# Optimization experiments

Hardware: AMD Instinct MI355X
Metric: run time of the kernel (lower is better)

Reference implementation:

```python
import jax, jax.numpy as jnp
import numpy as np

BW_MIN, BW_MAX, FLOAT_AMT, NEG_SLOPE = 0.1, 0.5, 0.1, 0.1


def setup_inputs() -> dict:
    key = jax.random.key(0)
    ks = jax.random.split(key, 24)
    B, S, IN_CH, GRID_CH, IC, DIR, OUT_CH = 8, 2000, 120, 64, 512, 4, 2
    NUM_BLOCK = 8
    n_layers = NUM_BLOCK - 2  # 6
    # grid coordinates: meshgrid over [0,10) with gap 0.1 -> 100x100 = 10000 pts
    gx = np.arange(0.0, 10.0, 0.1)
    gy = np.arange(0.0, 10.0, 0.1)
    GX, GY = np.meshgrid(gx, gy)
    grid_coors_xy = jnp.asarray(np.stack([GX.flatten(), GY.flatten()], axis=1), dtype=jnp.float32)  # [N,2]
    N = grid_coors_xy.shape[0]
    cat_ch = IN_CH + 2 * GRID_CH  # 248
    inp = {
        'input_stuff': jax.random.normal(ks[0], (B, S, IN_CH), jnp.float32),
        'sound_loc': jax.random.uniform(ks[1], (B, 4), jnp.float32) * 10.0,  # inside grid extent
        'grid_coors_xy': grid_coors_xy,
        'xy_offset': jnp.zeros((N, 2), jnp.float32),
        'bandwidths': jnp.full((N,), 0.25, jnp.float32),
        'grid_0': jax.random.normal(ks[2], (N, GRID_CH), jnp.float32) / np.sqrt(float(GRID_CH)),
        'proj_W': jax.random.normal(ks[3], (cat_ch, IC), jnp.float32) / np.sqrt(float(cat_ch)),
        'proj_b': jnp.zeros((IC,), jnp.float32),
        'res_W0': jax.random.normal(ks[4], (cat_ch, IC), jnp.float32) / np.sqrt(float(cat_ch)),
        'res_b0': jnp.zeros((IC,), jnp.float32),
        'res_W1': jax.random.normal(ks[5], (IC, IC), jnp.float32) / np.sqrt(float(IC)),
        'res_b1': jnp.zeros((IC,), jnp.float32),
        'layers_W': jax.random.normal(ks[6], (n_layers, IC, IC), jnp.float32) / np.sqrt(float(IC)),
        'layers_b': jnp.zeros((n_layers, IC), jnp.float32),
        'channels': jax.random.normal(ks[7], (NUM_BLOCK - 1, DIR, IC), jnp.float32) / np.sqrt(float(IC)),
        'out_W': jax.random.normal(ks[8], (IC, OUT_CH), jnp.float32) / np.sqrt(float(IC)),
        'out_b': jnp.zeros((OUT_CH,), jnp.float32),
    }
    return inp


def _leaky(x):
    return jax.nn.leaky_relu(x, NEG_SLOPE)


def _fit_predict(grid_pos, grid_feat, query_pos, bandwidths):
    d2 = jnp.sum((query_pos[:, None, :] - grid_pos[None, :, :]) ** 2, axis=-1)  # [B,N]
    w = jnp.exp(-d2 / (bandwidths[None, :] ** 2))                               # [B,N]
    w = w / jnp.sum(w, axis=-1, keepdims=True)
    return w @ grid_feat                                                        # [B,F]


def reference(input_stuff, sound_loc, grid_coors_xy, xy_offset, bandwidths, grid_0,
              proj_W, proj_b, res_W0, res_b0, res_W1, res_b1,
              layers_W, layers_b, channels, out_W, out_b):
    B, S = input_stuff.shape[0], input_stuff.shape[1]
    bw = jnp.clip(bandwidths, BW_MIN, BW_MAX)
    grid_baseline = grid_coors_xy + jnp.tanh(xy_offset) * FLOAT_AMT
    feat0 = _fit_predict(grid_baseline, grid_0, sound_loc[:, :2], bw)  # [B,64]
    feat1 = _fit_predict(grid_baseline, grid_0, sound_loc[:, 2:], bw)  # [B,64]
    total_grid = jnp.concatenate([feat0, feat1], axis=-1)              # [B,128]
    total_grid = jnp.broadcast_to(total_grid[:, None, :], (B, S, total_grid.shape[-1]))
    my_input = jnp.concatenate([total_grid, input_stuff], axis=-1)     # [B,S,248]

    # proj then broadcast over direction channels + learned channel embedding
    out = (my_input @ proj_W + proj_b)[:, :, None, :] + channels[0][None, None]  # [B,S,4,512]

    n_layers = layers_W.shape[0]
    half = n_layers // 2 - 1
    for k in range(n_layers):
        out = _leaky(out) @ layers_W[k] + layers_b[k] + channels[k + 1][None, None]
        if k == half:
            r = _leaky(my_input @ res_W0 + res_b0) @ res_W1 + res_b1  # [B,S,512]
            out = out + r[:, :, None, :]
    return out @ out_W + out_b  # [B,S,4,2]
```

## Files before the change

kernel.cpp:

```cpp
#include <hip/hip_runtime.h>
#include <hip/hip_bf16.h>

#define BB 8
#define SS 2000
#define IN_CH 120
#define GRID_CH 64
#define NPTS 10000
#define IC 512
#define DIRS 4
#define CATCH 248
#define CATPAD 256
#define NLAY 6
#define MROWS 16000
#define MROWS4 64000
#define NSLICE 16
#define PTS_PER_SLICE 625

typedef __bf16 bf16x8 __attribute__((ext_vector_type(8)));
typedef float f32x4 __attribute__((ext_vector_type(4)));

#define DEVI __device__ __forceinline__

DEVI unsigned short f2bf(float f) {
    __hip_bfloat16 h = __float2bfloat16(f);
    return __builtin_bit_cast(unsigned short, h);
}
DEVI float bf2f(unsigned short u) {
    unsigned int x = ((unsigned int)u) << 16;
    return __builtin_bit_cast(float, x);
}
DEVI float leaky(float x) { return x > 0.f ? x : 0.1f * x; }

DEVI void gload16(const void* g, void* l) {
    __builtin_amdgcn_global_load_lds(
        (const unsigned int __attribute__((address_space(1)))*)g,
        (unsigned int __attribute__((address_space(3)))*)l, 16, 0, 0);
}

static const size_t OFF_FEATS  = 0;
static const size_t OFF_PROJWT = 4096;
static const size_t OFF_RES0WT = 266240;
static const size_t OFF_RES1WT = 528384;
static const size_t OFF_LAYWT  = 1052672;
static const size_t OFF_MYIN   = 4198400;
static const size_t OFF_R0     = 12390400;
static const size_t OFF_R      = 28774400;
static const size_t OFF_A0     = 45158400;
static const size_t OFF_A1     = 110694400;

__global__ void wconv_k(const float* __restrict__ src, unsigned short* __restrict__ dst,
                        int K, int Kpad, int N, int total) {
    int idx = blockIdx.x * 256 + threadIdx.x;
    if (idx >= total) return;
    int k = idx % Kpad;
    int rem = idx / Kpad;
    int n = rem % N;
    int l = rem / N;
    float v = (k < K) ? src[((size_t)l * K + k) * N + n] : 0.f;
    dst[idx] = f2bf(v);
}

__global__ __launch_bounds__(256) void feats_part_k(
    const float* __restrict__ gxy, const float* __restrict__ goff,
    const float* __restrict__ bws, const float* __restrict__ g0,
    const float* __restrict__ sloc, float* __restrict__ partial) {
    int bq = blockIdx.x;
    int b = bq >> 1, q = bq & 1;
    float qx = sloc[b * 4 + q * 2 + 0];
    float qy = sloc[b * 4 + q * 2 + 1];
    int i0 = blockIdx.y * PTS_PER_SLICE;
    int iend = i0 + PTS_PER_SLICE;
    float swt = 0.f;
    float sf[64];
#pragma unroll
    for (int c = 0; c < 64; c++) sf[c] = 0.f;
    for (int i = i0 + threadIdx.x; i < iend; i += 256) {
        float gx = gxy[i * 2 + 0] + tanhf(goff[i * 2 + 0]) * 0.1f;
        float gy = gxy[i * 2 + 1] + tanhf(goff[i * 2 + 1]) * 0.1f;
        float bw = fminf(fmaxf(bws[i], 0.1f), 0.5f);
        float dx = qx - gx, dy = qy - gy;
        float w = expf(-(dx * dx + dy * dy) / (bw * bw));
        swt += w;
#pragma unroll
        for (int c = 0; c < 64; c++) sf[c] += w * g0[(size_t)i * 64 + c];
    }
#pragma unroll
    for (int c = 0; c < 64; c++)
        for (int o = 32; o; o >>= 1) sf[c] += __shfl_down(sf[c], o);
    for (int o = 32; o; o >>= 1) swt += __shfl_down(swt, o);
    __shared__ float red[4][65];
    int lane = threadIdx.x & 63, wv = threadIdx.x >> 6;
    if (lane == 0) {
#pragma unroll
        for (int c = 0; c < 64; c++) red[wv][c] = sf[c];
        red[wv][64] = swt;
    }
    __syncthreads();
    size_t base = (size_t)(blockIdx.y * 16 + bq) * 72;
    if (threadIdx.x < 64) {
        int c = threadIdx.x;
        partial[base + c] = red[0][c] + red[1][c] + red[2][c] + red[3][c];
        if (c == 0)
            partial[base + 64] = red[0][64] + red[1][64] + red[2][64] + red[3][64];
    }
}

__global__ __launch_bounds__(128) void feats_reduce_k(
    const float* __restrict__ partial, float* __restrict__ feats) {
    int bq = blockIdx.x;
    __shared__ float s[66];
    int t = threadIdx.x;
    if (t < 65) {
        float acc = 0.f;
        for (int sl = 0; sl < NSLICE; ++sl)
            acc += partial[(size_t)(sl * 16 + bq) * 72 + t];
        s[t] = acc;
    }
    __syncthreads();
    if (t < 64) {
        int b = bq >> 1, q = bq & 1;
        feats[b * 128 + q * 64 + t] = s[t] / s[64];
    }
}

__global__ void build_k(const float* __restrict__ feats, const float* __restrict__ inp,
                        unsigned short* __restrict__ dst) {
    int idx = blockIdx.x * 256 + threadIdx.x;
    int c = idx & 255;
    int m = idx >> 8;
    int b = m / SS;
    float v;
    if (c < 128) v = feats[b * 128 + c];
    else if (c < CATCH) v = inp[(size_t)m * IN_CH + (c - 128)];
    else v = 0.f;
    dst[idx] = f2bf(v);
}

template <int EPI>
__global__ __launch_bounds__(256) void gemm_k(
    const unsigned short* __restrict__ A, const unsigned short* __restrict__ BT,
    unsigned short* __restrict__ out, int K,
    const float* __restrict__ bias, const float* __restrict__ chan,
    const unsigned short* __restrict__ resid) {
    __shared__ unsigned short ldsA[8192];
    __shared__ unsigned short ldsB[8192];
    const int tid = threadIdx.x;
    const int lane = tid & 63, wv = tid >> 6;
    const int wm = wv >> 1, wn = wv & 1;
    const int c8 = lane >> 4;
    const int fr = lane & 15;

    int aoff[4][2], boff[4][2];
#pragma unroll
    for (int i = 0; i < 4; i++) {
        int ra = wm * 64 + i * 16 + fr;
        int rb = wn * 64 + i * 16 + fr;
#pragma unroll
        for (int h = 0; h < 2; h++) {
            int c = c8 + h * 4;
            aoff[i][h] = ra * 64 + ((c ^ (ra & 7)) << 3);
            boff[i][h] = rb * 64 + ((c ^ (rb & 7)) << 3);
        }
    }
    int ldso[4];
    size_t asrc[4];
    const unsigned short* Ab = A + (size_t)blockIdx.x * 128 * K;
    const unsigned short* Bb = BT + (size_t)blockIdx.y * 128 * K;
#pragma unroll
    for (int t = 0; t < 4; t++) {
        int o = t * 4096 + wv * 1024 + lane * 16;
        int r = o >> 7;
        int s = (o >> 4) & 7;
        int g = (s ^ (r & 7)) << 3;
        ldso[t] = o >> 1;
        asrc[t] = (size_t)r * K + g;
    }

    f32x4 acc[4][4];
#pragma unroll
    for (int i = 0; i < 4; i++)
#pragma unroll
        for (int j = 0; j < 4; j++) acc[i][j] = (f32x4)0.f;

    const int nK = K >> 6;
    for (int kt = 0; kt < nK; ++kt) {
        const int k0 = kt << 6;
        __syncthreads();
#pragma unroll
        for (int t = 0; t < 4; t++) gload16(Ab + asrc[t] + k0, &ldsA[ldso[t]]);
#pragma unroll
        for (int t = 0; t < 4; t++) gload16(Bb + asrc[t] + k0, &ldsB[ldso[t]]);
        __syncthreads();
#pragma unroll
        for (int h = 0; h < 2; h++) {
            bf16x8 av[4], bv[4];
#pragma unroll
            for (int i = 0; i < 4; i++) av[i] = *(const bf16x8*)&ldsA[aoff[i][h]];
#pragma unroll
            for (int j = 0; j < 4; j++) bv[j] = *(const bf16x8*)&ldsB[boff[j][h]];
#pragma unroll
            for (int i = 0; i < 4; i++)
#pragma unroll
                for (int j = 0; j < 4; j++)
                    acc[i][j] = __builtin_amdgcn_mfma_f32_16x16x32_bf16(av[i], bv[j], acc[i][j], 0, 0, 0);
        }
    }

    const int rbase = (lane >> 4) << 2;
    const size_t m0 = (size_t)blockIdx.x * 128;
    const int n0 = blockIdx.y * 128;
#pragma unroll
    for (int i = 0; i < 4; i++) {
#pragma unroll
        for (int j = 0; j < 4; j++) {
#pragma unroll
            for (int rg = 0; rg < 4; ++rg) {
                size_t m = m0 + wm * 64 + i * 16 + rbase + rg;
                int n = n0 + wn * 64 + j * 16 + fr;
                float v = acc[i][j][rg];
                if constexpr (EPI == 0) {
                    float v0 = v + bias[n];
#pragma unroll
                    for (int d = 0; d < 4; ++d) {
                        float u = v0 + chan[d * 512 + n];
                        out[(m * 4 + d) * 512 + n] = f2bf(leaky(u));
                    }
                } else if constexpr (EPI == 1 || EPI == 2 || EPI == 3) {
                    int d = (int)(m & 3);
                    float u = v + bias[n] + chan[d * 512 + n];
                    if constexpr (EPI == 2) u += bf2f(resid[(m >> 2) * 512 + n]);
                    out[m * 512 + n] = f2bf(EPI == 3 ? u : leaky(u));
                } else {
                    float u = v + bias[n];
                    out[m * 512 + n] = f2bf(EPI == 4 ? leaky(u) : u);
                }
            }
        }
    }
}

__global__ __launch_bounds__(256) void final_k(
    const unsigned short* __restrict__ A, const float* __restrict__ outW,
    const float* __restrict__ outb, float* __restrict__ out) {
    int gw = blockIdx.x * 4 + (threadIdx.x >> 6);
    int lane = threadIdx.x & 63;
    const unsigned short* row = A + (size_t)gw * 512;
    uint4 bits = *(const uint4*)(row + lane * 8);
    unsigned int ww[4] = {bits.x, bits.y, bits.z, bits.w};
    float s0 = 0.f, s1 = 0.f;
#pragma unroll
    for (int j = 0; j < 8; j++) {
        unsigned short u = (unsigned short)((ww[j >> 1] >> ((j & 1) * 16)) & 0xffff);
        float a = bf2f(u);
        int k = lane * 8 + j;
        s0 = fmaf(a, outW[k * 2 + 0], s0);
        s1 = fmaf(a, outW[k * 2 + 1], s1);
    }
    for (int o = 32; o; o >>= 1) {
        s0 += __shfl_down(s0, o);
        s1 += __shfl_down(s1, o);
    }
    if (lane == 0) {
        out[(size_t)gw * 2 + 0] = s0 + outb[0];
        out[(size_t)gw * 2 + 1] = s1 + outb[1];
    }
}

extern "C" void kernel_launch(void* const* d_in, const int* in_sizes, int n_in,
                              void* d_out, int out_size, void* d_ws, size_t ws_size,
                              hipStream_t stream) {
    const float* input_stuff = (const float*)d_in[0];
    const float* sound_loc   = (const float*)d_in[1];
    const float* grid_xy     = (const float*)d_in[2];
    const float* xy_offset   = (const float*)d_in[3];
    const float* bandwidths  = (const float*)d_in[4];
    const float* grid_0      = (const float*)d_in[5];
    const float* proj_W      = (const float*)d_in[6];
    const float* proj_b      = (const float*)d_in[7];
    const float* res_W0      = (const float*)d_in[8];
    const float* res_b0      = (const float*)d_in[9];
    const float* res_W1      = (const float*)d_in[10];
    const float* res_b1      = (const float*)d_in[11];
    const float* layers_W    = (const float*)d_in[12];
    const float* layers_b    = (const float*)d_in[13];
    const float* channels    = (const float*)d_in[14];
    const float* out_W       = (const float*)d_in[15];
    const float* out_b       = (const float*)d_in[16];

    char* ws = (char*)d_ws;
    float* feats            = (float*)(ws + OFF_FEATS);
    unsigned short* projWT  = (unsigned short*)(ws + OFF_PROJWT);
    unsigned short* res0WT  = (unsigned short*)(ws + OFF_RES0WT);
    unsigned short* res1WT  = (unsigned short*)(ws + OFF_RES1WT);
    unsigned short* layWT   = (unsigned short*)(ws + OFF_LAYWT);
    unsigned short* myin    = (unsigned short*)(ws + OFF_MYIN);
    unsigned short* R0      = (unsigned short*)(ws + OFF_R0);
    unsigned short* Rb      = (unsigned short*)(ws + OFF_R);
    unsigned short* A0      = (unsigned short*)(ws + OFF_A0);
    unsigned short* A1      = (unsigned short*)(ws + OFF_A1);
    float* partial          = (float*)(ws + OFF_A0);

    wconv_k<<<(512 * 256 + 255) / 256, 256, 0, stream>>>(proj_W, projWT, CATCH, CATPAD, IC, 512 * 256);
    wconv_k<<<(512 * 256 + 255) / 256, 256, 0, stream>>>(res_W0, res0WT, CATCH, CATPAD, IC, 512 * 256);
    wconv_k<<<(512 * 512 + 255) / 256, 256, 0, stream>>>(res_W1, res1WT, IC, IC, IC, 512 * 512);
    wconv_k<<<(6 * 512 * 512 + 255) / 256, 256, 0, stream>>>(layers_W, layWT, IC, IC, IC, 6 * 512 * 512);

    feats_part_k<<<dim3(16, NSLICE), 256, 0, stream>>>(grid_xy, xy_offset, bandwidths, grid_0, sound_loc, partial);
    feats_reduce_k<<<16, 128, 0, stream>>>(partial, feats);
    build_k<<<MROWS, 256, 0, stream>>>(feats, input_stuff, myin);

    dim3 g16(125, 4), g64(500, 4);
    gemm_k<0><<<g16, 256, 0, stream>>>(myin, projWT, A0, CATPAD, proj_b, channels, nullptr);
    gemm_k<4><<<g16, 256, 0, stream>>>(myin, res0WT, R0, CATPAD, res_b0, nullptr, nullptr);
    gemm_k<5><<<g16, 256, 0, stream>>>(R0, res1WT, Rb, IC, res_b1, nullptr, nullptr);
    gemm_k<1><<<g64, 256, 0, stream>>>(A0, layWT + 0 * 262144, A1, IC, layers_b + 0 * 512, channels + 1 * 2048, nullptr);
    gemm_k<1><<<g64, 256, 0, stream>>>(A1, layWT + 1 * 262144, A0, IC, layers_b + 1 * 512, channels + 2 * 2048, nullptr);
    gemm_k<2><<<g64, 256, 0, stream>>>(A0, layWT + 2 * 262144, A1, IC, layers_b + 2 * 512, channels + 3 * 2048, Rb);
    gemm_k<1><<<g64, 256, 0, stream>>>(A1, layWT + 3 * 262144, A0, IC, layers_b + 3 * 512, channels + 4 * 2048, nullptr);
    gemm_k<1><<<g64, 256, 0, stream>>>(A0, layWT + 4 * 262144, A1, IC, layers_b + 4 * 512, channels + 5 * 2048, nullptr);
    gemm_k<3><<<g64, 256, 0, stream>>>(A1, layWT + 5 * 262144, A0, IC, layers_b + 5 * 512, channels + 6 * 2048, nullptr);

    final_k<<<MROWS, 256, 0, stream>>>(A0, out_W, out_b, (float*)d_out);
}
```

Before: 501.3 us.

## Double-buffer GEMM LDS tiles and remap blocks for XCD-local tile reuse

The GEMM kernel now keeps two LDS buffers so the global-to-LDS load of the next K tile is issued before computing on the current one, leaving one barrier per iteration instead of two. The 2D grid is flattened to 1D and remapped so consecutive logical tiles, which share A rows across the four N tiles, land on the same XCD for better L2 reuse. LDS use doubles to 64KB per block, which may lower occupancy.

```diff
diff --git a/kernel.cpp b/kernel.cpp
--- a/kernel.cpp
+++ b/kernel.cpp
@@ -37,6 +37,15 @@
         (unsigned int __attribute__((address_space(3)))*)l, 16, 0, 0);
 }
 
+DEVI int xcd_swizzle() {
+    int nwg = (int)gridDim.x;
+    int orig = (int)blockIdx.x;
+    int q = nwg >> 3, r = nwg & 7;
+    int xcd = orig & 7, pos = orig >> 3;
+    int base = xcd < r ? xcd * (q + 1) : r * (q + 1) + (xcd - r) * q;
+    return base + pos;
+}
+
 static const size_t OFF_FEATS  = 0;
 static const size_t OFF_PROJWT = 4096;
 static const size_t OFF_RES0WT = 266240;
@@ -142,14 +151,16 @@
     unsigned short* __restrict__ out, int K,
     const float* __restrict__ bias, const float* __restrict__ chan,
     const unsigned short* __restrict__ resid) {
-    __shared__ unsigned short ldsA[8192];
-    __shared__ unsigned short ldsB[8192];
+    __shared__ __align__(16) unsigned short lds[2][2][8192];
     const int tid = threadIdx.x;
     const int lane = tid & 63, wv = tid >> 6;
     const int wm = wv >> 1, wn = wv & 1;
     const int c8 = lane >> 4;
     const int fr = lane & 15;
 
+    const int swz = xcd_swizzle();
+    const int bx = swz >> 2, by = swz & 3;
+
     int aoff[4][2], boff[4][2];
 #pragma unroll
     for (int i = 0; i < 4; i++) {
@@ -164,8 +175,8 @@
     }
     int ldso[4];
     size_t asrc[4];
-    const unsigned short* Ab = A + (size_t)blockIdx.x * 128 * K;
-    const unsigned short* Bb = BT + (size_t)blockIdx.y * 128 * K;
+    const unsigned short* Ab = A + (size_t)bx * 128 * K;
+    const unsigned short* Bb = BT + (size_t)by * 128 * K;
 #pragma unroll
     for (int t = 0; t < 4; t++) {
         int o = t * 4096 + wv * 1024 + lane * 16;
@@ -183,32 +194,47 @@
         for (int j = 0; j < 4; j++) acc[i][j] = (f32x4)0.f;
 
     const int nK = K >> 6;
+#pragma unroll
+    for (int t = 0; t < 4; t++) gload16(Ab + asrc[t], &lds[0][0][ldso[t]]);
+#pragma unroll
+    for (int t = 0; t < 4; t++) gload16(Bb + asrc[t], &lds[0][1][ldso[t]]);
+    asm volatile("s_waitcnt vmcnt(0)" ::: "memory");
+    __builtin_amdgcn_s_barrier();
+    __builtin_amdgcn_sched_barrier(0);
+
+    int buf = 0;
     for (int kt = 0; kt < nK; ++kt) {
-        const int k0 = kt << 6;
-        __syncthreads();
-#pragma unroll
-        for (int t = 0; t < 4; t++) gload16(Ab + asrc[t] + k0, &ldsA[ldso[t]]);
-#pragma unroll
-        for (int t = 0; t < 4; t++) gload16(Bb + asrc[t] + k0, &ldsB[ldso[t]]);
-        __syncthreads();
+        if (kt + 1 < nK) {
+            const int k1 = (kt + 1) << 6;
+#pragma unroll
+            for (int t = 0; t < 4; t++) gload16(Ab + asrc[t] + k1, &lds[buf ^ 1][0][ldso[t]]);
+#pragma unroll
+            for (int t = 0; t < 4; t++) gload16(Bb + asrc[t] + k1, &lds[buf ^ 1][1][ldso[t]]);
+        }
 #pragma unroll
         for (int h = 0; h < 2; h++) {
             bf16x8 av[4], bv[4];
 #pragma unroll
-            for (int i = 0; i < 4; i++) av[i] = *(const bf16x8*)&ldsA[aoff[i][h]];
-#pragma unroll
-            for (int j = 0; j < 4; j++) bv[j] = *(const bf16x8*)&ldsB[boff[j][h]];
+            for (int i = 0; i < 4; i++) av[i] = *(const bf16x8*)&lds[buf][0][aoff[i][h]];
+#pragma unroll
+            for (int j = 0; j < 4; j++) bv[j] = *(const bf16x8*)&lds[buf][1][boff[j][h]];
 #pragma unroll
             for (int i = 0; i < 4; i++)
 #pragma unroll
                 for (int j = 0; j < 4; j++)
                     acc[i][j] = __builtin_amdgcn_mfma_f32_16x16x32_bf16(av[i], bv[j], acc[i][j], 0, 0, 0);
         }
+        if (kt + 1 < nK) {
+            asm volatile("s_waitcnt vmcnt(0)" ::: "memory");
+            __builtin_amdgcn_s_barrier();
+            __builtin_amdgcn_sched_barrier(0);
+        }
+        buf ^= 1;
     }
 
     const int rbase = (lane >> 4) << 2;
-    const size_t m0 = (size_t)blockIdx.x * 128;
-    const int n0 = blockIdx.y * 128;
+    const size_t m0 = (size_t)bx * 128;
+    const int n0 = by * 128;
 #pragma unroll
     for (int i = 0; i < 4; i++) {
 #pragma unroll
@@ -309,16 +335,15 @@
     feats_reduce_k<<<16, 128, 0, stream>>>(partial, feats);
     build_k<<<MROWS, 256, 0, stream>>>(feats, input_stuff, myin);
 
-    dim3 g16(125, 4), g64(500, 4);
-    gemm_k<0><<<g16, 256, 0, stream>>>(myin, projWT, A0, CATPAD, proj_b, channels, nullptr);
-    gemm_k<4><<<g16, 256, 0, stream>>>(myin, res0WT, R0, CATPAD, res_b0, nullptr, nullptr);
-    gemm_k<5><<<g16, 256, 0, stream>>>(R0, res1WT, Rb, IC, res_b1, nullptr, nullptr);
-    gemm_k<1><<<g64, 256, 0, stream>>>(A0, layWT + 0 * 262144, A1, IC, layers_b + 0 * 512, channels + 1 * 2048, nullptr);
-    gemm_k<1><<<g64, 256, 0, stream>>>(A1, layWT + 1 * 262144, A0, IC, layers_b + 1 * 512, channels + 2 * 2048, nullptr);
-    gemm_k<2><<<g64, 256, 0, stream>>>(A0, layWT + 2 * 262144, A1, IC, layers_b + 2 * 512, channels + 3 * 2048, Rb);
-    gemm_k<1><<<g64, 256, 0, stream>>>(A1, layWT + 3 * 262144, A0, IC, layers_b + 3 * 512, channels + 4 * 2048, nullptr);
-    gemm_k<1><<<g64, 256, 0, stream>>>(A0, layWT + 4 * 262144, A1, IC, layers_b + 4 * 512, channels + 5 * 2048, nullptr);
-    gemm_k<3><<<g64, 256, 0, stream>>>(A1, layWT + 5 * 262144, A0, IC, layers_b + 5 * 512, channels + 6 * 2048, nullptr);
+    gemm_k<0><<<500, 256, 0, stream>>>(myin, projWT, A0, CATPAD, proj_b, channels, nullptr);
+    gemm_k<4><<<500, 256, 0, stream>>>(myin, res0WT, R0, CATPAD, res_b0, nullptr, nullptr);
+    gemm_k<5><<<500, 256, 0, stream>>>(R0, res1WT, Rb, IC, res_b1, nullptr, nullptr);
+    gemm_k<1><<<2000, 256, 0, stream>>>(A0, layWT + 0 * 262144, A1, IC, layers_b + 0 * 512, channels + 1 * 2048, nullptr);
+    gemm_k<1><<<2000, 256, 0, stream>>>(A1, layWT + 1 * 262144, A0, IC, layers_b + 1 * 512, channels + 2 * 2048, nullptr);
+    gemm_k<2><<<2000, 256, 0, stream>>>(A0, layWT + 2 * 262144, A1, IC, layers_b + 2 * 512, channels + 3 * 2048, Rb);
+    gemm_k<1><<<2000, 256, 0, stream>>>(A1, layWT + 3 * 262144, A0, IC, layers_b + 3 * 512, channels + 4 * 2048, nullptr);
+    gemm_k<1><<<2000, 256, 0, stream>>>(A0, layWT + 4 * 262144, A1, IC, layers_b + 4 * 512, channels + 5 * 2048, nullptr);
+    gemm_k<3><<<2000, 256, 0, stream>>>(A1, layWT + 5 * 262144, A0, IC, layers_b + 5 * 512, channels + 6 * 2048, nullptr);
 
     final_k<<<MROWS, 256, 0, stream>>>(A0, out_W, out_b, (float*)d_out);
 }
```

Result: faster. 403.8 us (-19.4%).

## Fuse entire MLP chain into one kernel keeping activations in LDS

Applied to the files above, without the earlier changes.

Replaces the build kernel, the nine separate GEMM launches and the final projection with a single fused kernel. Each 512-thread block owns 32 input rows (128 direction rows) and keeps its activation slab in 128KB of swizzled dynamic LDS across all layers. Weights are streamed straight from global or L2 into registers with double buffering, and only the residual branch is written to global memory. This removes the large global round-trips of activations between layers and the per-launch overhead. The cost is one block per CU from LDS usage, heavy register pressure from the 8x4 accumulator tiles, and no LDS reuse of the weight tiles.

```diff
diff --git a/kernel.cpp b/kernel.cpp
--- a/kernel.cpp
+++ b/kernel.cpp
@@ -4,20 +4,17 @@
 #define BB 8
 #define SS 2000
 #define IN_CH 120
-#define GRID_CH 64
 #define NPTS 10000
 #define IC 512
-#define DIRS 4
 #define CATCH 248
 #define CATPAD 256
-#define NLAY 6
 #define MROWS 16000
-#define MROWS4 64000
 #define NSLICE 16
 #define PTS_PER_SLICE 625
 
 typedef __bf16 bf16x8 __attribute__((ext_vector_type(8)));
 typedef float f32x4 __attribute__((ext_vector_type(4)));
+typedef unsigned short u16x8 __attribute__((ext_vector_type(8)));
 
 #define DEVI __device__ __forceinline__
 
@@ -30,23 +27,19 @@
     return __builtin_bit_cast(float, x);
 }
 DEVI float leaky(float x) { return x > 0.f ? x : 0.1f * x; }
-
-DEVI void gload16(const void* g, void* l) {
-    __builtin_amdgcn_global_load_lds(
-        (const unsigned int __attribute__((address_space(1)))*)g,
-        (unsigned int __attribute__((address_space(3)))*)l, 16, 0, 0);
-}
+DEVI unsigned int pk2(float a, float b) {
+    return (unsigned int)f2bf(a) | ((unsigned int)f2bf(b) << 16);
+}
+
+DEVI int slab_addr(int m, int ck) { return m * 1024 + ((ck ^ (m & 7)) << 4); }
 
 static const size_t OFF_FEATS  = 0;
 static const size_t OFF_PROJWT = 4096;
 static const size_t OFF_RES0WT = 266240;
 static const size_t OFF_RES1WT = 528384;
 static const size_t OFF_LAYWT  = 1052672;
-static const size_t OFF_MYIN   = 4198400;
-static const size_t OFF_R0     = 12390400;
-static const size_t OFF_R      = 28774400;
-static const size_t OFF_A0     = 45158400;
-static const size_t OFF_A1     = 110694400;
+static const size_t OFF_PART   = 4198400;
+static const size_t OFF_RG     = 12390400;
 
 __global__ void wconv_k(const float* __restrict__ src, unsigned short* __restrict__ dst,
                         int K, int Kpad, int N, int total) {
@@ -123,146 +116,237 @@
     }
 }
 
-__global__ void build_k(const float* __restrict__ feats, const float* __restrict__ inp,
-                        unsigned short* __restrict__ dst) {
-    int idx = blockIdx.x * 256 + threadIdx.x;
-    int c = idx & 255;
-    int m = idx >> 8;
-    int b = m / SS;
-    float v;
-    if (c < 128) v = feats[b * 128 + c];
-    else if (c < CATCH) v = inp[(size_t)m * IN_CH + (c - 128)];
-    else v = 0.f;
-    dst[idx] = f2bf(v);
-}
-
-template <int EPI>
-__global__ __launch_bounds__(256) void gemm_k(
-    const unsigned short* __restrict__ A, const unsigned short* __restrict__ BT,
-    unsigned short* __restrict__ out, int K,
-    const float* __restrict__ bias, const float* __restrict__ chan,
-    const unsigned short* __restrict__ resid) {
-    __shared__ unsigned short ldsA[8192];
-    __shared__ unsigned short ldsB[8192];
+
+template <int IM>
+DEVI void gemm_phase(const char* smem, int arow0, const unsigned short* __restrict__ BT,
+                     int Kpad, int nK, int wv, int lane, f32x4 (&acc)[IM][4]) {
+    const int fr = lane & 15, c8 = lane >> 4;
+#pragma unroll
+    for (int i = 0; i < IM; i++)
+#pragma unroll
+        for (int j = 0; j < 4; j++) acc[i][j] = (f32x4)0.f;
+
+    const unsigned short* Bw = BT + (size_t)(wv * 64 + fr) * Kpad + (size_t)c8 * 8;
+    const size_t jstep = (size_t)16 * Kpad;
+    uint4 bA[4], bB[4];
+
+#define LOADB(dst, kt)                                                        \
+    _Pragma("unroll") for (int j = 0; j < 4; j++)                             \
+        dst[j] = *(const uint4*)(Bw + (size_t)j * jstep + (size_t)(kt) * 32);
+
+#define COMPUTE(bb, kt)                                                       \
+    {                                                                         \
+        bf16x8 av[IM];                                                        \
+        _Pragma("unroll") for (int i = 0; i < IM; i++)                        \
+            av[i] = *(const bf16x8*)(smem + slab_addr(arow0 + i * 16 + fr, (kt) * 4 + c8)); \
+        _Pragma("unroll") for (int i = 0; i < IM; i++)                        \
+            _Pragma("unroll") for (int j = 0; j < 4; j++)                     \
+                acc[i][j] = __builtin_amdgcn_mfma_f32_16x16x32_bf16(          \
+                    av[i], __builtin_bit_cast(bf16x8, bb[j]), acc[i][j], 0, 0, 0); \
+    }
+
+    LOADB(bA, 0);
+    for (int kt = 0; kt < nK; kt += 2) {
+        LOADB(bB, kt + 1);
+        COMPUTE(bA, kt);
+        if (kt + 2 < nK) LOADB(bA, kt + 2);
+        COMPUTE(bB, kt + 1);
+    }
+#undef LOADB
+#undef COMPUTE
+}
+
+__global__ void __launch_bounds__(512, 2) fused_k(
+    const float* __restrict__ feats, const float* __restrict__ inp,
+    const unsigned short* __restrict__ projWT, const float* __restrict__ proj_b,
+    const unsigned short* __restrict__ res0WT, const float* __restrict__ res_b0,
+    const unsigned short* __restrict__ res1WT, const float* __restrict__ res_b1,
+    const unsigned short* __restrict__ layWT, const float* __restrict__ layers_b,
+    const float* __restrict__ channels, const float* __restrict__ outW,
+    const float* __restrict__ outb, unsigned short* __restrict__ r_g,
+    float* __restrict__ out) {
+    extern __shared__ __align__(16) char smem[];
     const int tid = threadIdx.x;
     const int lane = tid & 63, wv = tid >> 6;
-    const int wm = wv >> 1, wn = wv & 1;
-    const int c8 = lane >> 4;
     const int fr = lane & 15;
-
-    int aoff[4][2], boff[4][2];
-#pragma unroll
-    for (int i = 0; i < 4; i++) {
-        int ra = wm * 64 + i * 16 + fr;
-        int rb = wn * 64 + i * 16 + fr;
-#pragma unroll
-        for (int h = 0; h < 2; h++) {
-            int c = c8 + h * 4;
-            aoff[i][h] = ra * 64 + ((c ^ (ra & 7)) << 3);
-            boff[i][h] = rb * 64 + ((c ^ (rb & 7)) << 3);
-        }
-    }
-    int ldso[4];
-    size_t asrc[4];
-    const unsigned short* Ab = A + (size_t)blockIdx.x * 128 * K;
-    const unsigned short* Bb = BT + (size_t)blockIdx.y * 128 * K;
-#pragma unroll
-    for (int t = 0; t < 4; t++) {
-        int o = t * 4096 + wv * 1024 + lane * 16;
-        int r = o >> 7;
-        int s = (o >> 4) & 7;
-        int g = (s ^ (r & 7)) << 3;
-        ldso[t] = o >> 1;
-        asrc[t] = (size_t)r * K + g;
-    }
-
-    f32x4 acc[4][4];
-#pragma unroll
-    for (int i = 0; i < 4; i++)
-#pragma unroll
-        for (int j = 0; j < 4; j++) acc[i][j] = (f32x4)0.f;
-
-    const int nK = K >> 6;
-    for (int kt = 0; kt < nK; ++kt) {
-        const int k0 = kt << 6;
+    const int hh = lane >> 4;
+    const size_t base0 = (size_t)blockIdx.x * 32;
+
+    {
+        int r = tid >> 4;
+        int cp = tid & 15;
+        size_t mrow = base0 + r;
+        int b = (int)(mrow / SS);
+        const float* fb = feats + b * 128;
+#pragma unroll
+        for (int h = 0; h < 2; ++h) {
+            int ck = cp * 2 + h;
+            unsigned int w[4];
+#pragma unroll
+            for (int p = 0; p < 4; ++p) {
+                int k = ck * 8 + p * 2;
+                float v0 = (k < 128) ? fb[k] : (k < CATCH ? inp[mrow * IN_CH + (k - 128)] : 0.f);
+                k++;
+                float v1 = (k < 128) ? fb[k] : (k < CATCH ? inp[mrow * IN_CH + (k - 128)] : 0.f);
+                w[p] = pk2(v0, v1);
+            }
+            *(uint4*)(smem + slab_addr(r, ck)) = make_uint4(w[0], w[1], w[2], w[3]);
+        }
+    }
+    __syncthreads();
+
+    f32x4 acc2[2][4];
+
+    gemm_phase<2>(smem, 0, res0WT, CATPAD, 8, wv, lane, acc2);
+#pragma unroll
+    for (int i = 0; i < 2; i++) {
+#pragma unroll
+        for (int j = 0; j < 4; j++) {
+            int n = wv * 64 + j * 16 + fr;
+            float bn = res_b0[n];
+            float v[4];
+#pragma unroll
+            for (int rg = 0; rg < 4; rg++) v[rg] = leaky(acc2[i][j][rg] + bn);
+            unsigned int p01 = pk2(v[0], v[1]), p23 = pk2(v[2], v[3]);
+            unsigned int q01 = (unsigned int)__shfl_xor((int)p01, 1);
+            unsigned int q23 = (unsigned int)__shfl_xor((int)p23, 1);
+            int np = n & ~1;
+            int mrow = 32 + i * 16 + hh * 4;
+            if (!(fr & 1)) {
+                *(unsigned int*)(smem + slab_addr(mrow + 0, np >> 3) + (np & 7) * 2) =
+                    (p01 & 0xffffu) | ((q01 & 0xffffu) << 16);
+                *(unsigned int*)(smem + slab_addr(mrow + 1, np >> 3) + (np & 7) * 2) =
+                    (p01 >> 16) | (q01 & 0xffff0000u);
+            } else {
+                *(unsigned int*)(smem + slab_addr(mrow + 2, np >> 3) + (np & 7) * 2) =
+                    (q23 & 0xffffu) | ((p23 & 0xffffu) << 16);
+                *(unsigned int*)(smem + slab_addr(mrow + 3, np >> 3) + (np & 7) * 2) =
+                    (q23 >> 16) | (p23 & 0xffff0000u);
+            }
+        }
+    }
+    __syncthreads();
+
+    gemm_phase<2>(smem, 32, res1WT, IC, 16, wv, lane, acc2);
+#pragma unroll
+    for (int i = 0; i < 2; i++) {
+#pragma unroll
+        for (int j = 0; j < 4; j++) {
+            int n = wv * 64 + j * 16 + fr;
+            float bn = res_b1[n];
+#pragma unroll
+            for (int rg = 0; rg < 4; rg++) {
+                int mb = i * 16 + hh * 4 + rg;
+                r_g[(base0 + mb) * IC + n] = f2bf(acc2[i][j][rg] + bn);
+            }
+        }
+    }
+
+    gemm_phase<2>(smem, 0, projWT, CATPAD, 8, wv, lane, acc2);
+    __syncthreads();
+#pragma unroll
+    for (int i = 0; i < 2; i++) {
+#pragma unroll
+        for (int j = 0; j < 4; j++) {
+            int n = wv * 64 + j * 16 + fr;
+            float bn = proj_b[n];
+            float ch[4];
+#pragma unroll
+            for (int d = 0; d < 4; d++) ch[d] = channels[d * 512 + n];
+            int np = n & ~1;
+#pragma unroll
+            for (int rg = 0; rg < 4; rg++) {
+                int mb = i * 16 + hh * 4 + rg;
+                float vb = acc2[i][j][rg] + bn;
+                float v[4];
+#pragma unroll
+                for (int d = 0; d < 4; d++) v[d] = leaky(vb + ch[d]);
+                unsigned int p01 = pk2(v[0], v[1]), p23 = pk2(v[2], v[3]);
+                unsigned int q01 = (unsigned int)__shfl_xor((int)p01, 1);
+                unsigned int q23 = (unsigned int)__shfl_xor((int)p23, 1);
+                int m4 = mb * 4;
+                if (!(fr & 1)) {
+                    *(unsigned int*)(smem + slab_addr(m4 + 0, np >> 3) + (np & 7) * 2) =
+                        (p01 & 0xffffu) | ((q01 & 0xffffu) << 16);
+                    *(unsigned int*)(smem + slab_addr(m4 + 1, np >> 3) + (np & 7) * 2) =
+                        (p01 >> 16) | (q01 & 0xffff0000u);
+                } else {
+                    *(unsigned int*)(smem + slab_addr(m4 + 2, np >> 3) + (np & 7) * 2) =
+                        (q23 & 0xffffu) | ((p23 & 0xffffu) << 16);
+                    *(unsigned int*)(smem + slab_addr(m4 + 3, np >> 3) + (np & 7) * 2) =
+                        (q23 >> 16) | (p23 & 0xffff0000u);
+                }
+            }
+        }
+    }
+    __syncthreads();
+
+    f32x4 acc8[8][4];
+    for (int l = 0; l < 6; ++l) {
+        gemm_phase<8>(smem, 0, layWT + (size_t)l * 262144, IC, 16, wv, lane, acc8);
         __syncthreads();
-#pragma unroll
-        for (int t = 0; t < 4; t++) gload16(Ab + asrc[t] + k0, &ldsA[ldso[t]]);
-#pragma unroll
-        for (int t = 0; t < 4; t++) gload16(Bb + asrc[t] + k0, &ldsB[ldso[t]]);
+        const float* bias = layers_b + l * 512;
+        const float* chan = channels + (l + 1) * 2048;
+        const bool use_r = (l == 2);
+        const bool do_lk = (l != 5);
+#pragma unroll
+        for (int i = 0; i < 8; i++) {
+#pragma unroll
+            for (int j = 0; j < 4; j++) {
+                int n = wv * 64 + j * 16 + fr;
+                float bn = bias[n];
+                float rv = 0.f;
+                if (use_r) rv = bf2f(r_g[(base0 + 4 * i + hh) * IC + n]);
+                float v[4];
+#pragma unroll
+                for (int rg = 0; rg < 4; rg++) {
+                    float u = acc8[i][j][rg] + bn + chan[rg * 512 + n] + rv;
+                    v[rg] = do_lk ? leaky(u) : u;
+                }
+                unsigned int p01 = pk2(v[0], v[1]), p23 = pk2(v[2], v[3]);
+                unsigned int q01 = (unsigned int)__shfl_xor((int)p01, 1);
+                unsigned int q23 = (unsigned int)__shfl_xor((int)p23, 1);
+                int np = n & ~1;
+                int m = i * 16 + hh * 4;
+                if (!(fr & 1)) {
+                    *(unsigned int*)(smem + slab_addr(m + 0, np >> 3) + (np & 7) * 2) =
+                        (p01 & 0xffffu) | ((q01 & 0xffffu) << 16);
+                    *(unsigned int*)(smem + slab_addr(m + 1, np >> 3) + (np & 7) * 2) =
+                        (p01 >> 16) | (q01 & 0xffff0000u);
+                } else {
+                    *(unsigned int*)(smem + slab_addr(m + 2, np >> 3) + (np & 7) * 2) =
+                        (q23 & 0xffffu) | ((p23 & 0xffffu) << 16);
+                    *(unsigned int*)(smem + slab_addr(m + 3, np >> 3) + (np & 7) * 2) =
+                        (q23 >> 16) | (p23 & 0xffff0000u);
+                }
+            }
+        }
         __syncthreads();
-#pragma unroll
-        for (int h = 0; h < 2; h++) {
-            bf16x8 av[4], bv[4];
-#pragma unroll
-            for (int i = 0; i < 4; i++) av[i] = *(const bf16x8*)&ldsA[aoff[i][h]];
-#pragma unroll
-            for (int j = 0; j < 4; j++) bv[j] = *(const bf16x8*)&ldsB[boff[j][h]];
-#pragma unroll
-            for (int i = 0; i < 4; i++)
-#pragma unroll
-                for (int j = 0; j < 4; j++)
-                    acc[i][j] = __builtin_amdgcn_mfma_f32_16x16x32_bf16(av[i], bv[j], acc[i][j], 0, 0, 0);
-        }
-    }
-
-    const int rbase = (lane >> 4) << 2;
-    const size_t m0 = (size_t)blockIdx.x * 128;
-    const int n0 = blockIdx.y * 128;
-#pragma unroll
-    for (int i = 0; i < 4; i++) {
-#pragma unroll
-        for (int j = 0; j < 4; j++) {
-#pragma unroll
-            for (int rg = 0; rg < 4; ++rg) {
-                size_t m = m0 + wm * 64 + i * 16 + rbase + rg;
-                int n = n0 + wn * 64 + j * 16 + fr;
-                float v = acc[i][j][rg];
-                if constexpr (EPI == 0) {
-                    float v0 = v + bias[n];
-#pragma unroll
-                    for (int d = 0; d < 4; ++d) {
-                        float u = v0 + chan[d * 512 + n];
-                        out[(m * 4 + d) * 512 + n] = f2bf(leaky(u));
-                    }
-                } else if constexpr (EPI == 1 || EPI == 2 || EPI == 3) {
-                    int d = (int)(m & 3);
-                    float u = v + bias[n] + chan[d * 512 + n];
-                    if constexpr (EPI == 2) u += bf2f(resid[(m >> 2) * 512 + n]);
-                    out[m * 512 + n] = f2bf(EPI == 3 ? u : leaky(u));
-                } else {
-                    float u = v + bias[n];
-                    out[m * 512 + n] = f2bf(EPI == 4 ? leaky(u) : u);
-                }
-            }
-        }
-    }
-}
-
-__global__ __launch_bounds__(256) void final_k(
-    const unsigned short* __restrict__ A, const float* __restrict__ outW,
-    const float* __restrict__ outb, float* __restrict__ out) {
-    int gw = blockIdx.x * 4 + (threadIdx.x >> 6);
-    int lane = threadIdx.x & 63;
-    const unsigned short* row = A + (size_t)gw * 512;
-    uint4 bits = *(const uint4*)(row + lane * 8);
-    unsigned int ww[4] = {bits.x, bits.y, bits.z, bits.w};
-    float s0 = 0.f, s1 = 0.f;
-#pragma unroll
-    for (int j = 0; j < 8; j++) {
-        unsigned short u = (unsigned short)((ww[j >> 1] >> ((j & 1) * 16)) & 0xffff);
-        float a = bf2f(u);
-        int k = lane * 8 + j;
-        s0 = fmaf(a, outW[k * 2 + 0], s0);
-        s1 = fmaf(a, outW[k * 2 + 1], s1);
-    }
-    for (int o = 32; o; o >>= 1) {
-        s0 += __shfl_down(s0, o);
-        s1 += __shfl_down(s1, o);
-    }
-    if (lane == 0) {
-        out[(size_t)gw * 2 + 0] = s0 + outb[0];
-        out[(size_t)gw * 2 + 1] = s1 + outb[1];
+    }
+
+    {
+        int m = wv * 16 + (lane >> 2);
+        int q = lane & 3;
+        float s0 = 0.f, s1 = 0.f;
+#pragma unroll
+        for (int ck = 0; ck < 16; ++ck) {
+            u16x8 a = *(const u16x8*)(smem + slab_addr(m, q * 16 + ck));
+#pragma unroll
+            for (int e = 0; e < 8; ++e) {
+                int k = (q * 16 + ck) * 8 + e;
+                float av = bf2f(a[e]);
+                float2 wp = *(const float2*)&outW[k * 2];
+                s0 = fmaf(av, wp.x, s0);
+                s1 = fmaf(av, wp.y, s1);
+            }
+        }
+        s0 += __shfl_down(s0, 2); s0 += __shfl_down(s0, 1);
+        s1 += __shfl_down(s1, 2); s1 += __shfl_down(s1, 1);
+        if (q == 0) {
+            size_t gm = (size_t)blockIdx.x * 128 + m;
+            out[gm * 2 + 0] = s0 + outb[0];
+            out[gm * 2 + 1] = s1 + outb[1];
+        }
     }
 }
 
@@ -293,12 +377,8 @@
     unsigned short* res0WT  = (unsigned short*)(ws + OFF_RES0WT);
     unsigned short* res1WT  = (unsigned short*)(ws + OFF_RES1WT);
     unsigned short* layWT   = (unsigned short*)(ws + OFF_LAYWT);
-    unsigned short* myin    = (unsigned short*)(ws + OFF_MYIN);
-    unsigned short* R0      = (unsigned short*)(ws + OFF_R0);
-    unsigned short* Rb      = (unsigned short*)(ws + OFF_R);
-    unsigned short* A0      = (unsigned short*)(ws + OFF_A0);
-    unsigned short* A1      = (unsigned short*)(ws + OFF_A1);
-    float* partial          = (float*)(ws + OFF_A0);
+    float* partial          = (float*)(ws + OFF_PART);
+    unsigned short* r_g     = (unsigned short*)(ws + OFF_RG);
 
     wconv_k<<<(512 * 256 + 255) / 256, 256, 0, stream>>>(proj_W, projWT, CATCH, CATPAD, IC, 512 * 256);
     wconv_k<<<(512 * 256 + 255) / 256, 256, 0, stream>>>(res_W0, res0WT, CATCH, CATPAD, IC, 512 * 256);
@@ -307,18 +387,14 @@
 
     feats_part_k<<<dim3(16, NSLICE), 256, 0, stream>>>(grid_xy, xy_offset, bandwidths, grid_0, sound_loc, partial);
     feats_reduce_k<<<16, 128, 0, stream>>>(partial, feats);
-    build_k<<<MROWS, 256, 0, stream>>>(feats, input_stuff, myin);
-
-    dim3 g16(125, 4), g64(500, 4);
-    gemm_k<0><<<g16, 256, 0, stream>>>(myin, projWT, A0, CATPAD, proj_b, channels, nullptr);
-    gemm_k<4><<<g16, 256, 0, stream>>>(myin, res0WT, R0, CATPAD, res_b0, nullptr, nullptr);
-    gemm_k<5><<<g16, 256, 0, stream>>>(R0, res1WT, Rb, IC, res_b1, nullptr, nullptr);
-    gemm_k<1><<<g64, 256, 0, stream>>>(A0, layWT + 0 * 262144, A1, IC, layers_b + 0 * 512, channels + 1 * 2048, nullptr);
-    gemm_k<1><<<g64, 256, 0, stream>>>(A1, layWT + 1 * 262144, A0, IC, layers_b + 1 * 512, channels + 2 * 2048, nullptr);
-    gemm_k<2><<<g64, 256, 0, stream>>>(A0, layWT + 2 * 262144, A1, IC, layers_b + 2 * 512, channels + 3 * 2048, Rb);
-    gemm_k<1><<<g64, 256, 0, stream>>>(A1, layWT + 3 * 262144, A0, IC, layers_b + 3 * 512, channels + 4 * 2048, nullptr);
-    gemm_k<1><<<g64, 256, 0, stream>>>(A0, layWT + 4 * 262144, A1, IC, layers_b + 4 * 512, channels + 5 * 2048, nullptr);
-    gemm_k<3><<<g64, 256, 0, stream>>>(A1, layWT + 5 * 262144, A0, IC, layers_b + 5 * 512, channels + 6 * 2048, nullptr);
-
-    final_k<<<MROWS, 256, 0, stream>>>(A0, out_W, out_b, (float*)d_out);
-}
+
+    static int smem_set = 0;
+    if (!smem_set) {
+        hipFuncSetAttribute((const void*)fused_k,
+                            hipFuncAttributeMaxDynamicSharedMemorySize, 131072);
+        smem_set = 1;
+    }
+    fused_k<<<500, 512, 131072, stream>>>(
+        feats, input_stuff, projWT, proj_b, res0WT, res_b0, res1WT, res_b1,
+        layWT, layers_b, channels, out_W, out_b, r_g, (float*)d_out);
+}
```

After: 713.3 us. 42.3% more time.
